# Optimization experiments

Measured on AMD Instinct MI355X. Metric: run time of the kernel, lower is better.

Reference implementation:

```python
import jax, jax.numpy as jnp
import numpy as np

WS = 7
B, Dd, Hh, Wd, C, NH = 1, 28, 28, 28, 384, 12

def _rel_index(ws):
    coords = np.stack(np.meshgrid(np.arange(ws), np.arange(ws), np.arange(ws), indexing='ij'))
    cf = coords.reshape(3, -1)
    rel = (cf[:, :, None] - cf[:, None, :]).transpose(1, 2, 0) + (ws - 1)
    rel[:, :, 0] *= (2 * ws - 1) ** 2
    rel[:, :, 1] *= (2 * ws - 1)
    return rel.sum(-1)  # (ws^3, ws^3)

REL_IDX = _rel_index(WS)

def setup_inputs():
    key = jax.random.key(0)
    ks = jax.random.split(key, 8)
    L = Dd * Hh * Wd
    s = 0.02
    return {
        'skip': jax.random.normal(ks[0], (B, L, C), jnp.float32),
        'x_up': jax.random.normal(ks[1], (B, L, C), jnp.float32),
        'D': Dd, 'H': Hh, 'W': Wd,
        'ln1_g': jnp.ones((C,), jnp.float32), 'ln1_b': jnp.zeros((C,), jnp.float32),
        'kv_w': jax.random.normal(ks[2], (C, 2 * C), jnp.float32) * s,
        'kv_b': jnp.zeros((2 * C,), jnp.float32),
        'rpb': jax.random.normal(ks[3], ((2 * WS - 1) ** 3, NH), jnp.float32) * s,
        'proj_w': jax.random.normal(ks[4], (C, C), jnp.float32) * s,
        'proj_b': jnp.zeros((C,), jnp.float32),
        'ln2_g': jnp.ones((C,), jnp.float32), 'ln2_b': jnp.zeros((C,), jnp.float32),
        'mlp_w1': jax.random.normal(ks[5], (C, 4 * C), jnp.float32) * s,
        'mlp_b1': jnp.zeros((4 * C,), jnp.float32),
        'mlp_w2': jax.random.normal(ks[6], (4 * C, C), jnp.float32) * s,
        'mlp_b2': jnp.zeros((C,), jnp.float32),
    }

def _ln(x, g, b):
    m = jnp.mean(x, -1, keepdims=True)
    v = jnp.mean(jnp.square(x - m), -1, keepdims=True)
    return (x - m) * jax.lax.rsqrt(v + 1e-5) * g + b

def _win_part(x):
    b, d, h, w, c = x.shape
    x = x.reshape(b, d // WS, WS, h // WS, WS, w // WS, WS, c)
    return x.transpose(0, 1, 3, 5, 2, 4, 6, 7).reshape(-1, WS ** 3, c)

def _win_rev(x, b, d, h, w):
    c = x.shape[-1]
    x = x.reshape(b, d // WS, h // WS, w // WS, WS, WS, WS, c)
    return x.transpose(0, 1, 4, 2, 5, 3, 6, 7).reshape(b, d, h, w, c)

def reference(skip, x_up, D, H, W, ln1_g, ln1_b, kv_w, kv_b, rpb, proj_w, proj_b, ln2_g, ln2_b, mlp_w1, mlp_b1, mlp_w2, mlp_b2):
    b, L, c = skip.shape
    x = x_up + skip  # wrapper residual; shortcut of the inner block
    # inner block was built with shift_size=0 -> no cyclic shift, attn_mask unused
    sk = _win_part(_ln(skip, ln1_g, ln1_b).reshape(b, D, H, W, c))   # (nW, N, C) -> K,V source
    qx = _win_part(_ln(x_up, ln1_g, ln1_b).reshape(b, D, H, W, c))   # (nW, N, C) -> Q source
    nW, N, _ = sk.shape
    hd = c // NH
    kv = (sk @ kv_w + kv_b).reshape(nW, N, 2, NH, hd)
    k, v = kv[:, :, 0], kv[:, :, 1]                  # (nW, N, NH, hd)
    q = qx.reshape(nW, N, NH, hd) * (hd ** -0.5)     # no q projection in WindowAttention_kv
    attn = jnp.einsum('wqhd,wkhd->whqk', q, k)
    bias = rpb[REL_IDX.reshape(-1)].reshape(N, N, NH).transpose(2, 0, 1)
    attn = jax.nn.softmax(attn + bias[None], axis=-1)
    o = jnp.einsum('whqk,wkhd->wqhd', attn, v).reshape(nW, N, c)
    o = o @ proj_w + proj_b
    o = _win_rev(o, b, D, H, W).reshape(b, L, c)
    x = x + o
    h1 = jax.nn.gelu(_ln(x, ln2_g, ln2_b) @ mlp_w1 + mlp_b1)
    x = x + h1 @ mlp_w2 + mlp_b2
    return x
```

## Files before the change

kernel.cpp:

```cpp
#include <hip/hip_runtime.h>
#include <hip/hip_bf16.h>
#include <cstdint>

typedef unsigned short u16;
typedef short s16x8 __attribute__((ext_vector_type(8)));
typedef short s16x4 __attribute__((ext_vector_type(4)));
typedef float f32x4 __attribute__((ext_vector_type(4)));

#define C_DIM 384
#define NHEAD 12
#define HD    32
#define NTOK  343
#define NWIN  64
#define LTOT  21952
#define SIDE  28

__device__ __forceinline__ float u2f(u16 u) {
    return __uint_as_float(((unsigned int)u) << 16);
}
__device__ __forceinline__ u16 f2b(float f) {
    unsigned int u = __float_as_uint(f);
    return (u16)((u + 0x7fffu + ((u >> 16) & 1u)) >> 16);
}
__device__ __forceinline__ float exp2_hw(float x) {
    float r;
    asm("v_exp_f32 %0, %1" : "=v"(r) : "v"(x));
    return r;
}
__device__ __forceinline__ unsigned int pk_bf16(float lo, float hi) {
    unsigned int r;
    asm("v_cvt_pk_bf16_f32 %0, %1, %2" : "=v"(r) : "v"(lo), "v"(hi));
    return r;
}
__device__ __forceinline__ float gelu_fast(float x) {
    float e = exp2_hw(-2.3022083f * (x + 0.044715f * x * x * x));
    return x * __builtin_amdgcn_rcpf(1.f + e);
}

__global__ __launch_bounds__(256) void k_wt(
    const float* __restrict__ W, u16* __restrict__ Wt, int K, int N)
{
    __shared__ float T[64][65];
    int k0 = blockIdx.x * 64, n0 = blockIdx.y * 64;
    int t = threadIdx.x;
    int c = t & 63, rg = t >> 6;
#pragma unroll
    for (int i = 0; i < 16; i++) {
        int r = rg * 16 + i;
        T[r][c] = W[(size_t)(k0 + r) * N + n0 + c];
    }
    __syncthreads();
    int k = t & 63, ng = t >> 6;
#pragma unroll
    for (int i = 0; i < 16; i++) {
        int n = ng * 16 + i;
        Wt[(size_t)(n0 + n) * K + k0 + k] = f2b(T[k][n]);
    }
}

__global__ __launch_bounds__(256) void k_wt_pi(
    const float* __restrict__ W, u16* __restrict__ Wt, int K, int N)
{
    __shared__ float T[64][65];
    int k0 = blockIdx.x * 64, n0 = blockIdx.y * 64;
    int t = threadIdx.x;
    int c = t & 63, rg = t >> 6;
#pragma unroll
    for (int i = 0; i < 16; i++) {
        int r = rg * 16 + i;
        T[r][c] = W[(size_t)(k0 + r) * N + n0 + c];
    }
    __syncthreads();
    int k = t & 63, ng = t >> 6;
    int kg = k0 + k;
    int j = kg & 127, ct = j >> 4, nn = j & 15;
    int kp = (kg & ~127) | ((ct >> 1) << 5) | (nn << 1) | (ct & 1);
#pragma unroll
    for (int i = 0; i < 16; i++) {
        int n = ng * 16 + i;
        Wt[(size_t)(n0 + n) * K + kp] = f2b(T[k][n]);
    }
}

__global__ __launch_bounds__(256) void k_bias(
    const float* __restrict__ rpb, u16* __restrict__ biasPl)
{
    int h = blockIdx.x, q = blockIdx.y;
    int qc = min(q, NTOK - 1);
    int qz = qc / 49, qrem = qc % 49, qy = qrem / 7, qx = qrem % 7;
    int cq = qz * 169 + qy * 13 + qx;
    u16* dst = biasPl + ((size_t)h * 352 + q) * 352;
    for (int k = threadIdx.x; k < 352; k += 256) {
        int kc = min(k, NTOK - 1);
        int kz = kc / 49, krem = kc % 49, ky = krem / 7, kx = krem % 7;
        int ck = kz * 169 + ky * 13 + kx;
        dst[k] = f2b(rpb[(size_t)(cq - ck + 1098) * NHEAD + h] * 1.4426950408889634f);
    }
}

#define QSCALE 0.2550348772f

__global__ __launch_bounds__(256) void k_lnprep(
    const float* __restrict__ skip, const float* __restrict__ xup,
    const float* __restrict__ g, const float* __restrict__ bta,
    u16* __restrict__ skW, u16* __restrict__ qW, u16* __restrict__ res)
{
    int t = blockIdx.x * 4 + (threadIdx.x >> 6);
    int lane = threadIdx.x & 63;
    const float* ps = skip + (size_t)t * C_DIM;
    const float* px = xup + (size_t)t * C_DIM;
    float vs[6], vx[6];
    float s1 = 0.f, s2 = 0.f, x1 = 0.f, x2 = 0.f;
#pragma unroll
    for (int j = 0; j < 6; j++) {
        float a = ps[lane + j * 64];
        float b = px[lane + j * 64];
        vs[j] = a; vx[j] = b;
        s1 += a; s2 += a * a; x1 += b; x2 += b * b;
    }
#pragma unroll
    for (int off = 32; off; off >>= 1) {
        s1 += __shfl_xor(s1, off);
        s2 += __shfl_xor(s2, off);
        x1 += __shfl_xor(x1, off);
        x2 += __shfl_xor(x2, off);
    }
    float ms = s1 * (1.f / 384.f), mx = x1 * (1.f / 384.f);
    float rs = rsqrtf(fmaxf(s2 * (1.f / 384.f) - ms * ms, 0.f) + 1e-5f);
    float rx = rsqrtf(fmaxf(x2 * (1.f / 384.f) - mx * mx, 0.f) + 1e-5f);
    int d = t / 784, rem = t % 784, hh = rem / 28, ww = rem % 28;
    int win = (d / 7) * 16 + (hh / 7) * 4 + (ww / 7);
    int n = (d % 7) * 49 + (hh % 7) * 7 + (ww % 7);
    size_t dst = ((size_t)(win * NTOK + n)) * C_DIM + lane;
    size_t td  = (size_t)t * C_DIM + lane;
#pragma unroll
    for (int j = 0; j < 6; j++) {
        int c = lane + j * 64;
        float gg = g[c], bb = bta[c];
        skW[dst + j * 64] = f2b((vs[j] - ms) * rs * gg + bb);
        qW[dst + j * 64]  = f2b(((vx[j] - mx) * rx * gg + bb) * QSCALE);
        res[td + j * 64]  = f2b(vs[j] + vx[j]);
    }
}

__global__ __launch_bounds__(256) void k_ln2(
    const u16* __restrict__ x2, const float* __restrict__ g,
    const float* __restrict__ bta, u16* __restrict__ lnx)
{
    int t = blockIdx.x * 4 + (threadIdx.x >> 6);
    int lane = threadIdx.x & 63;
    const u16* p = x2 + (size_t)t * C_DIM;
    float v[6];
    float s1 = 0.f, s2 = 0.f;
#pragma unroll
    for (int j = 0; j < 6; j++) {
        float a = u2f(p[lane + j * 64]);
        v[j] = a; s1 += a; s2 += a * a;
    }
#pragma unroll
    for (int off = 32; off; off >>= 1) {
        s1 += __shfl_xor(s1, off);
        s2 += __shfl_xor(s2, off);
    }
    float m = s1 * (1.f / 384.f);
    float r = rsqrtf(fmaxf(s2 * (1.f / 384.f) - m * m, 0.f) + 1e-5f);
    size_t dst = (size_t)t * C_DIM + lane;
#pragma unroll
    for (int j = 0; j < 6; j++) {
        int c = lane + j * 64;
        lnx[dst + j * 64] = f2b((v[j] - m) * r * g[c] + bta[c]);
    }
}

#define BPAD 40

__device__ __forceinline__ void gemm128(
    const u16* __restrict__ A, const u16* __restrict__ Bt, int K, int M,
    int rowBase, int colBase, int tid,
    u16 (*As)[BPAD], u16 (*Bs)[BPAD], f32x4 acc[4][4])
{
    const int sr  = tid >> 2;
    const int scg = (tid & 3) << 3;
    const int lane = tid & 63, wv = tid >> 6;
    const int m16 = lane & 15, quad = lane >> 4;
    const int wr = (wv >> 1) << 6, wc = (wv & 1) << 6;

    int ra0 = min(rowBase + sr, M - 1);
    int ra1 = min(rowBase + 64 + sr, M - 1);
    const u16* pa0 = A + (size_t)ra0 * K + scg;
    const u16* pa1 = A + (size_t)ra1 * K + scg;
    const u16* pb0 = Bt + (size_t)(colBase + sr) * K + scg;
    const u16* pb1 = Bt + (size_t)(colBase + 64 + sr) * K + scg;

    uint4 a0 = *(const uint4*)pa0, a1 = *(const uint4*)pa1;
    uint4 b0 = *(const uint4*)pb0, b1 = *(const uint4*)pb1;

    for (int kk = 0; kk < K; kk += 32) {
        *(uint4*)&As[sr][scg]      = a0;
        *(uint4*)&As[64 + sr][scg] = a1;
        *(uint4*)&Bs[sr][scg]      = b0;
        *(uint4*)&Bs[64 + sr][scg] = b1;
        __syncthreads();
        if (kk + 32 < K) {
            a0 = *(const uint4*)(pa0 + kk + 32);
            a1 = *(const uint4*)(pa1 + kk + 32);
            b0 = *(const uint4*)(pb0 + kk + 32);
            b1 = *(const uint4*)(pb1 + kk + 32);
        }
        s16x8 af[4], bf[4];
#pragma unroll
        for (int rt = 0; rt < 4; rt++)
            af[rt] = *(const s16x8*)&As[wr + rt * 16 + m16][quad * 8];
#pragma unroll
        for (int bt = 0; bt < 4; bt++)
            bf[bt] = *(const s16x8*)&Bs[wc + bt * 16 + m16][quad * 8];
#pragma unroll
        for (int rt = 0; rt < 4; rt++)
#pragma unroll
        for (int bt = 0; bt < 4; bt++)
            acc[rt][bt] = __builtin_amdgcn_mfma_f32_16x16x32_bf16(af[rt], bf[bt], acc[rt][bt], 0, 0, 0);
        __syncthreads();
    }
}

__device__ __forceinline__ void gemm64_db(
    const u16* __restrict__ A, const u16* __restrict__ Bt, int K, int M,
    int rowBase, int colBase, int tid,
    u16 (*As)[BPAD], u16 (*Bs)[BPAD], f32x4 acc[4][2])
{
    const int sr  = tid >> 2;
    const int scg = (tid & 3) << 3;
    const int lane = tid & 63, wv = tid >> 6;
    const int m16 = lane & 15, quad = lane >> 4;
    const int wc = wv << 5;

    int ra = min(rowBase + sr, M - 1);
    const u16* pa  = A + (size_t)ra * K + scg;
    const u16* pb0 = Bt + (size_t)(colBase + sr) * K + scg;
    const u16* pb1 = Bt + (size_t)(colBase + 64 + sr) * K + scg;

    uint4 aA = *(const uint4*)pa,        bA0 = *(const uint4*)pb0,        bA1 = *(const uint4*)pb1;
    uint4 aB = *(const uint4*)(pa + 32), bB0 = *(const uint4*)(pb0 + 32), bB1 = *(const uint4*)(pb1 + 32);

    *(uint4*)&As[sr][scg]      = aA;
    *(uint4*)&Bs[sr][scg]      = bA0;
    *(uint4*)&Bs[64 + sr][scg] = bA1;
    if (64 < K) {
        aA  = *(const uint4*)(pa + 64);
        bA0 = *(const uint4*)(pb0 + 64);
        bA1 = *(const uint4*)(pb1 + 64);
    }
    __syncthreads();

    for (int kk = 0; kk < K; kk += 64) {
        *(uint4*)&As[64 + sr][scg]  = aB;
        *(uint4*)&Bs[128 + sr][scg] = bB0;
        *(uint4*)&Bs[192 + sr][scg] = bB1;
        if (kk + 96 < K) {
            aB  = *(const uint4*)(pa  + kk + 96);
            bB0 = *(const uint4*)(pb0 + kk + 96);
            bB1 = *(const uint4*)(pb1 + kk + 96);
        }
        {
            s16x8 af[4], bf[2];
#pragma unroll
            for (int rt = 0; rt < 4; rt++)
                af[rt] = *(const s16x8*)&As[rt * 16 + m16][quad * 8];
#pragma unroll
            for (int bt = 0; bt < 2; bt++)
                bf[bt] = *(const s16x8*)&Bs[wc + bt * 16 + m16][quad * 8];
#pragma unroll
            for (int rt = 0; rt < 4; rt++)
#pragma unroll
            for (int bt = 0; bt < 2; bt++)
                acc[rt][bt] = __builtin_amdgcn_mfma_f32_16x16x32_bf16(af[rt], bf[bt], acc[rt][bt], 0, 0, 0);
        }
        __syncthreads();
        if (kk + 64 < K) {
            *(uint4*)&As[sr][scg]      = aA;
            *(uint4*)&Bs[sr][scg]      = bA0;
            *(uint4*)&Bs[64 + sr][scg] = bA1;
        }
        if (kk + 128 < K) {
            aA  = *(const uint4*)(pa  + kk + 128);
            bA0 = *(const uint4*)(pb0 + kk + 128);
            bA1 = *(const uint4*)(pb1 + kk + 128);
        }
        {
            s16x8 af[4], bf[2];
#pragma unroll
            for (int rt = 0; rt < 4; rt++)
                af[rt] = *(const s16x8*)&As[64 + rt * 16 + m16][quad * 8];
#pragma unroll
            for (int bt = 0; bt < 2; bt++)
                bf[bt] = *(const s16x8*)&Bs[128 + wc + bt * 16 + m16][quad * 8];
#pragma unroll
            for (int rt = 0; rt < 4; rt++)
#pragma unroll
            for (int bt = 0; bt < 2; bt++)
                acc[rt][bt] = __builtin_amdgcn_mfma_f32_16x16x32_bf16(af[rt], bf[bt], acc[rt][bt], 0, 0, 0);
        }
        __syncthreads();
    }
}

#define EPI_SETUP \
    int lane = tid & 63, wv = tid >> 6, quad = lane >> 4, n16 = lane & 15;

__global__ __launch_bounds__(256) void k_gemm_kv(
    const u16* __restrict__ A, const u16* __restrict__ Wt, const float* __restrict__ bias,
    u16* __restrict__ Kb, u16* __restrict__ Vb)
{
    __shared__ __align__(16) u16 As[128][BPAD];
    __shared__ __align__(16) u16 Bs[128][BPAD];
    f32x4 acc[4][4] = {};
    int tid = threadIdx.x;
    int rowBase = blockIdx.x * 128, colBase = blockIdx.y * 128;
    gemm128(A, Wt, 384, LTOT, rowBase, colBase, tid, As, Bs, acc);
    EPI_SETUP
    int wr = (wv >> 1) << 6, wc = (wv & 1) << 6;
#pragma unroll
    for (int bt = 0; bt < 4; bt++) {
        int col = colBase + wc + bt * 16 + n16;
        float bcol = bias[col];
        int isv = col >= 384;
        int remc = col - (isv ? 384 : 0);
        int hh = remc >> 5, dd = remc & 31;
#pragma unroll
        for (int rt = 0; rt < 4; rt++)
#pragma unroll
        for (int reg = 0; reg < 4; reg++) {
            int r = rowBase + wr + rt * 16 + quad * 4 + reg;
            if (r < LTOT) {
                int w = r / NTOK, nn = r % NTOK;
                size_t dst = ((size_t)((w * NHEAD + hh) * NTOK + nn)) * HD + dd;
                (isv ? Vb : Kb)[dst] = f2b(acc[rt][bt][reg] + bcol);
            }
        }
    }
}

__global__ __launch_bounds__(256) void k_gemm_proj(
    const u16* __restrict__ A, const u16* __restrict__ Wt, const float* __restrict__ bias,
    const u16* __restrict__ res, u16* __restrict__ x2)
{
    __shared__ __align__(16) u16 As[128][BPAD];
    __shared__ __align__(16) u16 Bs[256][BPAD];
    f32x4 acc[4][2] = {};
    int tid = threadIdx.x;
    int rowBase = blockIdx.x * 64, colBase = blockIdx.y * 128;
    gemm64_db(A, Wt, 384, LTOT, rowBase, colBase, tid, As, Bs, acc);
    EPI_SETUP
    int wc = wv << 5;
#pragma unroll
    for (int bt = 0; bt < 2; bt++) {
        int col = colBase + wc + bt * 16 + n16;
        float bcol = bias[col];
#pragma unroll
        for (int rt = 0; rt < 4; rt++)
#pragma unroll
        for (int reg = 0; reg < 4; reg++) {
            int r = rowBase + rt * 16 + quad * 4 + reg;
            if (r < LTOT) {
                size_t idx = (size_t)r * C_DIM + col;
                x2[idx] = f2b(acc[rt][bt][reg] + bcol + u2f(res[idx]));
            }
        }
    }
}

__global__ __launch_bounds__(256) void k_gemm_mlp1(
    const u16* __restrict__ A, const u16* __restrict__ Wt, const float* __restrict__ bias,
    u16* __restrict__ h1c, int rowOfs)
{
    __shared__ __align__(16) u16 As[128][BPAD];
    __shared__ __align__(16) u16 Bs[128][BPAD];
    f32x4 acc[4][4] = {};
    int tid = threadIdx.x;
    int rowBase = rowOfs + blockIdx.x * 128, colBase = blockIdx.y * 128;
    gemm128(A, Wt, 384, LTOT, rowBase, colBase, tid, As, Bs, acc);
    EPI_SETUP
    int wr = (wv >> 1) << 6;
#pragma unroll
    for (int p2 = 0; p2 < 2; p2++) {
        int p = (wv & 1) * 2 + p2;
        int col0 = colBase + p * 32 + n16;
        int col1 = col0 + 16;
        float bc0 = bias[col0], bc1 = bias[col1];
        int dcol = colBase + p * 32 + 2 * n16;
#pragma unroll
        for (int rt = 0; rt < 4; rt++)
#pragma unroll
        for (int reg = 0; reg < 4; reg++) {
            int r = rowBase + wr + rt * 16 + quad * 4 + reg;
            if (r < LTOT) {
                size_t rl = (size_t)(r - rowOfs);
                float v0 = gelu_fast(acc[rt][2 * p2][reg] + bc0);
                float v1 = gelu_fast(acc[rt][2 * p2 + 1][reg] + bc1);
                *(unsigned int*)&h1c[rl * 1536 + dcol] = pk_bf16(v0, v1);
            }
        }
    }
}

__global__ __launch_bounds__(256) void k_gemm_mlp2(
    const u16* __restrict__ A, const u16* __restrict__ Wt, const float* __restrict__ bias,
    const u16* __restrict__ x2, float* __restrict__ out, int rowOfs, int chunkRows)
{
    __shared__ __align__(16) u16 As[128][BPAD];
    __shared__ __align__(16) u16 Bs[256][BPAD];
    f32x4 acc[4][2] = {};
    int tid = threadIdx.x;
    int rowBase = blockIdx.x * 64, colBase = blockIdx.y * 128;
    gemm64_db(A, Wt, 1536, chunkRows, rowBase, colBase, tid, As, Bs, acc);
    EPI_SETUP
    int wc = wv << 5;
#pragma unroll
    for (int bt = 0; bt < 2; bt++) {
        int col = colBase + wc + bt * 16 + n16;
        float bcol = bias[col];
#pragma unroll
        for (int rt = 0; rt < 4; rt++)
#pragma unroll
        for (int reg = 0; reg < 4; reg++) {
            int rl = rowBase + rt * 16 + quad * 4 + reg;
            int rg = rowOfs + rl;
            if (rl < chunkRows && rg < LTOT) {
                size_t idx = (size_t)rg * C_DIM + col;
                out[idx] = acc[rt][bt][reg] + bcol + u2f(x2[idx]);
            }
        }
    }
}

#define VP  360
#define PBS 36

__global__ __launch_bounds__(256, 2) void k_attn(
    const u16* __restrict__ qW, const u16* __restrict__ Kb, const u16* __restrict__ Vb,
    const u16* __restrict__ biasPl, u16* __restrict__ oT)
{
    __shared__ __align__(16) u16 Vt[32 * VP];
    __shared__ __align__(16) u16 Pb[4 * 16 * PBS];

    const int h = blockIdx.x, w = blockIdx.y;
    const int tid = threadIdx.x;
    const int lane = tid & 63, wv = tid >> 6;
    const int m16 = lane & 15, quad = lane >> 4;
    const size_t base = ((size_t)(w * NHEAD + h)) * NTOK * HD;
    const u16* Kg = Kb + base;

    for (int t = tid; t < 704; t += 256) {
        int dg = t / 176, rem = t - dg * 176;
        int kb = rem >> 4, j = rem & 15;
        int n0 = kb * 32 + j, n1 = n0 + 16;
        uint4 uA = make_uint4(0, 0, 0, 0), uB = make_uint4(0, 0, 0, 0);
        if (n0 < NTOK) uA = *(const uint4*)(Vb + base + n0 * HD + dg * 8);
        if (n1 < NTOK) uB = *(const uint4*)(Vb + base + n1 * HD + dg * 8);
        int d0 = dg * 8, colu = kb * 32 + 2 * j;
        unsigned int pk0 = (uA.x & 0xffffu) | (uB.x << 16);
        unsigned int pk1 = (uA.x >> 16)     | (uB.x & 0xffff0000u);
        unsigned int pk2 = (uA.y & 0xffffu) | (uB.y << 16);
        unsigned int pk3 = (uA.y >> 16)     | (uB.y & 0xffff0000u);
        unsigned int pk4 = (uA.z & 0xffffu) | (uB.z << 16);
        unsigned int pk5 = (uA.z >> 16)     | (uB.z & 0xffff0000u);
        unsigned int pk6 = (uA.w & 0xffffu) | (uB.w << 16);
        unsigned int pk7 = (uA.w >> 16)     | (uB.w & 0xffff0000u);
        *(unsigned int*)&Vt[(d0 + 0) * VP + colu] = pk0;
        *(unsigned int*)&Vt[(d0 + 1) * VP + colu] = pk1;
        *(unsigned int*)&Vt[(d0 + 2) * VP + colu] = pk2;
        *(unsigned int*)&Vt[(d0 + 3) * VP + colu] = pk3;
        *(unsigned int*)&Vt[(d0 + 4) * VP + colu] = pk4;
        *(unsigned int*)&Vt[(d0 + 5) * VP + colu] = pk5;
        *(unsigned int*)&Vt[(d0 + 6) * VP + colu] = pk6;
        *(unsigned int*)&Vt[(d0 + 7) * VP + colu] = pk7;
    }
    __syncthreads();

    u16* myP = Pb + wv * 16 * PBS;

    for (int qt = wv; qt < 22; qt += 4) {
        int qbase = qt * 16;
        int qrow = min(qbase + m16, NTOK - 1);
        s16x8 qf = *(const s16x8*)(qW + ((size_t)(w * NTOK + qrow)) * C_DIM
                                       + h * HD + quad * 8);
        const u16* bp = biasPl + ((size_t)h * 352 + qbase + quad * 4) * 352;

        f32x4 S0[11], S1[11];
        float mx[4] = {-1e30f, -1e30f, -1e30f, -1e30f};

#pragma unroll
        for (int ks = 0; ks < 11; ks++) {
            int kbase = ks * 32;
            int kt0 = kbase + m16, kt1 = kt0 + 16;
            s16x8 kf0 = *(const s16x8*)(Kg + (size_t)kt0 * HD + quad * 8);
            s16x8 kf1 = *(const s16x8*)(Kg + (size_t)kt1 * HD + quad * 8);
            f32x4 c0, c1;
#pragma unroll
            for (int i = 0; i < 4; i++) {
                c0[i] = u2f(bp[i * 352 + kt0]);
                c1[i] = u2f(bp[i * 352 + kt1]);
            }
            f32x4 sA = __builtin_amdgcn_mfma_f32_16x16x32_bf16(qf, kf0, c0, 0, 0, 0);
            f32x4 sB = __builtin_amdgcn_mfma_f32_16x16x32_bf16(qf, kf1, c1, 0, 0, 0);
            bool k1ok = (ks < 10) || (kt1 < NTOK);
#pragma unroll
            for (int i = 0; i < 4; i++) {
                float sa = sA[i];
                float sb = k1ok ? sB[i] : -1e30f;
                S0[ks][i] = sa;
                S1[ks][i] = sb;
                mx[i] = fmaxf(mx[i], fmaxf(sa, sb));
            }
        }
#pragma unroll
        for (int i = 0; i < 4; i++) {
            float v = mx[i];
            v = fmaxf(v, __shfl_xor(v, 1));
            v = fmaxf(v, __shfl_xor(v, 2));
            v = fmaxf(v, __shfl_xor(v, 4));
            v = fmaxf(v, __shfl_xor(v, 8));
            mx[i] = v;
        }

        f32x4 O0 = {}, O1 = {};
        float l[4] = {};
#pragma unroll
        for (int ks = 0; ks < 11; ks++) {
            int kbase = ks * 32;
#pragma unroll
            for (int i = 0; i < 4; i++) {
                float pa = exp2_hw(S0[ks][i] - mx[i]);
                float pb = exp2_hw(S1[ks][i] - mx[i]);
                l[i] += pa + pb;
                *(unsigned int*)&myP[(quad * 4 + i) * PBS + 2 * m16] = pk_bf16(pa, pb);
            }
            s16x4 plo = *(const s16x4*)&myP[m16 * PBS + quad * 8];
            s16x4 phi = *(const s16x4*)&myP[m16 * PBS + quad * 8 + 4];
            s16x8 pf  = __builtin_shufflevector(plo, phi, 0, 1, 2, 3, 4, 5, 6, 7);
            s16x8 vf0 = *(const s16x8*)&Vt[m16 * VP + kbase + quad * 8];
            s16x8 vf1 = *(const s16x8*)&Vt[(16 + m16) * VP + kbase + quad * 8];
            O0 = __builtin_amdgcn_mfma_f32_16x16x32_bf16(pf, vf0, O0, 0, 0, 0);
            O1 = __builtin_amdgcn_mfma_f32_16x16x32_bf16(pf, vf1, O1, 0, 0, 0);
        }
#pragma unroll
        for (int i = 0; i < 4; i++) {
            float v = l[i];
            v += __shfl_xor(v, 1);
            v += __shfl_xor(v, 2);
            v += __shfl_xor(v, 4);
            v += __shfl_xor(v, 8);
            l[i] = v;
        }

        int wd = w >> 4, wh = (w >> 2) & 3, wwi = w & 3;
#pragma unroll
        for (int i = 0; i < 4; i++) {
            int q = qbase + quad * 4 + i;
            if (q < NTOK) {
                float rl = __builtin_amdgcn_rcpf(l[i]);
                int qz = q / 49, qrem = q % 49, qy = qrem / 7, qx = qrem % 7;
                size_t tok = ((size_t)(wd * 7 + qz) * SIDE + (wh * 7 + qy)) * SIDE
                             + (wwi * 7 + qx);
                u16* op = oT + tok * C_DIM + h * HD;
                op[m16]      = f2b(O0[i] * rl);
                op[16 + m16] = f2b(O1[i] * rl);
            }
        }
    }
}

extern "C" void kernel_launch(void* const* d_in, const int* in_sizes, int n_in,
                              void* d_out, int out_size, void* d_ws, size_t ws_size,
                              hipStream_t stream)
{
    const float* skip = (const float*)d_in[0];
    const float* xup  = (const float*)d_in[1];
    const float* ln1g = (const float*)d_in[5];
    const float* ln1b = (const float*)d_in[6];
    const float* kvw  = (const float*)d_in[7];
    const float* kvb  = (const float*)d_in[8];
    const float* rpb  = (const float*)d_in[9];
    const float* pw   = (const float*)d_in[10];
    const float* pb   = (const float*)d_in[11];
    const float* ln2g = (const float*)d_in[12];
    const float* ln2b = (const float*)d_in[13];
    const float* w1   = (const float*)d_in[14];
    const float* b1   = (const float*)d_in[15];
    const float* w2   = (const float*)d_in[16];
    const float* b2   = (const float*)d_in[17];
    float* out = (float*)d_out;

    char* ws = (char*)d_ws;
    const size_t BUFB = (size_t)LTOT * C_DIM * 2;
    const size_t WTB  = 589824 + 294912 + 1179648 + 1179648;
    const size_t BIASB = (size_t)NHEAD * 352 * 352 * 2;
    u16* skW = (u16*)(ws);
    u16* qW  = (u16*)(ws + BUFB);
    u16* Kb  = (u16*)(ws + 2 * BUFB);
    u16* Vb  = (u16*)(ws + 3 * BUFB);
    u16* oT  = (u16*)(ws);
    u16* x2  = (u16*)(ws + BUFB);
    u16* lnx = (u16*)(ws + 2 * BUFB);
    char* wt = ws + 4 * BUFB;
    u16* kvWt = (u16*)(wt);
    u16* pWt  = (u16*)(wt + 589824);
    u16* w1t  = (u16*)(wt + 589824 + 294912);
    u16* w2t  = (u16*)(wt + 589824 + 294912 + 1179648);
    u16* biasPl = (u16*)(wt + WTB);
    u16* res  = (u16*)d_out;

    const size_t used = 4 * BUFB + WTB + BIASB;
    const size_t blkBytes = 128 * 1536 * 2;
    size_t tailCap = (ws_size > used) ? (ws_size - used) / blkBytes : 0;
    int chunkBlocks;
    u16* h1c;
    if (tailCap >= 43) {
        chunkBlocks = tailCap < 172 ? (int)tailCap : 172;
        h1c = (u16*)(ws + used);
    } else {
        chunkBlocks = 42;
        h1c = (u16*)(ws + 3 * BUFB);
    }

    k_wt<<<dim3(6, 12), 256, 0, stream>>>(kvw, kvWt, 384, 768);
    k_wt<<<dim3(6, 6),  256, 0, stream>>>(pw,  pWt,  384, 384);
    k_wt<<<dim3(6, 24), 256, 0, stream>>>(w1,  w1t,  384, 1536);
    k_wt_pi<<<dim3(24, 6), 256, 0, stream>>>(w2, w2t, 1536, 384);
    k_bias<<<dim3(NHEAD, 352), 256, 0, stream>>>(rpb, biasPl);

    k_lnprep<<<LTOT / 4, 256, 0, stream>>>(skip, xup, ln1g, ln1b, skW, qW, res);
    k_gemm_kv<<<dim3(172, 6), 256, 0, stream>>>(skW, kvWt, kvb, Kb, Vb);
    k_attn<<<dim3(NHEAD, NWIN), 256, 0, stream>>>(qW, Kb, Vb, biasPl, oT);
    k_gemm_proj<<<dim3(343, 3), 256, 0, stream>>>(oT, pWt, pb, res, x2);
    k_ln2<<<LTOT / 4, 256, 0, stream>>>(x2, ln2g, ln2b, lnx);
    for (int b0 = 0; b0 < 172; b0 += chunkBlocks) {
        int nb = (172 - b0) < chunkBlocks ? (172 - b0) : chunkBlocks;
        int rowOfs = b0 * 128;
        int chunkRows = nb * 128;
        if (rowOfs + chunkRows > LTOT) chunkRows = LTOT - rowOfs;
        int nb64 = (chunkRows + 63) / 64;
        k_gemm_mlp1<<<dim3(nb, 12), 256, 0, stream>>>(lnx, w1t, b1, h1c, rowOfs);
        k_gemm_mlp2<<<dim3(nb64, 3), 256, 0, stream>>>(h1c, w2t, b2, x2, out, rowOfs, chunkRows);
    }
}
```

Baseline: 423.1 us.

## Stage GEMM tiles via direct global-to-LDS loads with double buffering

```diff
diff --git a/kernel.cpp b/kernel.cpp
--- a/kernel.cpp
+++ b/kernel.cpp
@@ -35,6 +35,11 @@
 __device__ __forceinline__ float gelu_fast(float x) {
     float e = exp2_hw(-2.3022083f * (x + 0.044715f * x * x * x));
     return x * __builtin_amdgcn_rcpf(1.f + e);
+}
+__device__ __forceinline__ void gl16(const u16* g, u16* l) {
+    __builtin_amdgcn_global_load_lds(
+        (const __attribute__((address_space(1))) void*)g,
+        (__attribute__((address_space(3))) void*)l, 16, 0, 0);
 }
 
 __global__ __launch_bounds__(256) void k_wt(
@@ -172,12 +177,10 @@
     }
 }
 
-#define BPAD 40
-
-__device__ __forceinline__ void gemm128(
+__device__ __forceinline__ void gemm128_gl(
     const u16* __restrict__ A, const u16* __restrict__ Bt, int K, int M,
     int rowBase, int colBase, int tid,
-    u16 (*As)[BPAD], u16 (*Bs)[BPAD], f32x4 acc[4][4])
+    u16 (*As)[32], u16 (*Bs)[32], f32x4 acc[4][4])
 {
     const int sr  = tid >> 2;
     const int scg = (tid & 3) << 3;
@@ -192,41 +195,44 @@
     const u16* pb0 = Bt + (size_t)(colBase + sr) * K + scg;
     const u16* pb1 = Bt + (size_t)(colBase + 64 + sr) * K + scg;
 
-    uint4 a0 = *(const uint4*)pa0, a1 = *(const uint4*)pa1;
-    uint4 b0 = *(const uint4*)pb0, b1 = *(const uint4*)pb1;
-
+    u16* a0d = &As[0][0]  + wv * 512;
+    u16* a1d = &As[64][0] + wv * 512;
+    u16* b0d = &Bs[0][0]  + wv * 512;
+    u16* b1d = &Bs[64][0] + wv * 512;
+
+    gl16(pa0, a0d); gl16(pa1, a1d); gl16(pb0, b0d); gl16(pb1, b1d);
+    __syncthreads();
+
+    int buf = 0;
     for (int kk = 0; kk < K; kk += 32) {
-        *(uint4*)&As[sr][scg]      = a0;
-        *(uint4*)&As[64 + sr][scg] = a1;
-        *(uint4*)&Bs[sr][scg]      = b0;
-        *(uint4*)&Bs[64 + sr][scg] = b1;
-        __syncthreads();
         if (kk + 32 < K) {
-            a0 = *(const uint4*)(pa0 + kk + 32);
-            a1 = *(const uint4*)(pa1 + kk + 32);
-            b0 = *(const uint4*)(pb0 + kk + 32);
-            b1 = *(const uint4*)(pb1 + kk + 32);
+            int nb = (buf ^ 1) * 4096;
+            gl16(pa0 + kk + 32, a0d + nb);
+            gl16(pa1 + kk + 32, a1d + nb);
+            gl16(pb0 + kk + 32, b0d + nb);
+            gl16(pb1 + kk + 32, b1d + nb);
         }
         s16x8 af[4], bf[4];
 #pragma unroll
         for (int rt = 0; rt < 4; rt++)
-            af[rt] = *(const s16x8*)&As[wr + rt * 16 + m16][quad * 8];
+            af[rt] = *(const s16x8*)&As[buf * 128 + wr + rt * 16 + m16][quad * 8];
 #pragma unroll
         for (int bt = 0; bt < 4; bt++)
-            bf[bt] = *(const s16x8*)&Bs[wc + bt * 16 + m16][quad * 8];
+            bf[bt] = *(const s16x8*)&Bs[buf * 128 + wc + bt * 16 + m16][quad * 8];
 #pragma unroll
         for (int rt = 0; rt < 4; rt++)
 #pragma unroll
         for (int bt = 0; bt < 4; bt++)
             acc[rt][bt] = __builtin_amdgcn_mfma_f32_16x16x32_bf16(af[rt], bf[bt], acc[rt][bt], 0, 0, 0);
         __syncthreads();
-    }
-}
-
-__device__ __forceinline__ void gemm64_db(
+        buf ^= 1;
+    }
+}
+
+__device__ __forceinline__ void gemm64_gl(
     const u16* __restrict__ A, const u16* __restrict__ Bt, int K, int M,
     int rowBase, int colBase, int tid,
-    u16 (*As)[BPAD], u16 (*Bs)[BPAD], f32x4 acc[4][2])
+    u16 (*As)[32], u16 (*Bs)[32], f32x4 acc[4][2])
 {
     const int sr  = tid >> 2;
     const int scg = (tid & 3) << 3;
@@ -239,68 +245,36 @@
     const u16* pb0 = Bt + (size_t)(colBase + sr) * K + scg;
     const u16* pb1 = Bt + (size_t)(colBase + 64 + sr) * K + scg;
 
-    uint4 aA = *(const uint4*)pa,        bA0 = *(const uint4*)pb0,        bA1 = *(const uint4*)pb1;
-    uint4 aB = *(const uint4*)(pa + 32), bB0 = *(const uint4*)(pb0 + 32), bB1 = *(const uint4*)(pb1 + 32);
-
-    *(uint4*)&As[sr][scg]      = aA;
-    *(uint4*)&Bs[sr][scg]      = bA0;
-    *(uint4*)&Bs[64 + sr][scg] = bA1;
-    if (64 < K) {
-        aA  = *(const uint4*)(pa + 64);
-        bA0 = *(const uint4*)(pb0 + 64);
-        bA1 = *(const uint4*)(pb1 + 64);
-    }
+    u16* ad  = &As[0][0]  + wv * 512;
+    u16* b0d = &Bs[0][0]  + wv * 512;
+    u16* b1d = &Bs[64][0] + wv * 512;
+
+    gl16(pa, ad); gl16(pb0, b0d); gl16(pb1, b1d);
     __syncthreads();
 
-    for (int kk = 0; kk < K; kk += 64) {
-        *(uint4*)&As[64 + sr][scg]  = aB;
-        *(uint4*)&Bs[128 + sr][scg] = bB0;
-        *(uint4*)&Bs[192 + sr][scg] = bB1;
-        if (kk + 96 < K) {
-            aB  = *(const uint4*)(pa  + kk + 96);
-            bB0 = *(const uint4*)(pb0 + kk + 96);
-            bB1 = *(const uint4*)(pb1 + kk + 96);
-        }
-        {
-            s16x8 af[4], bf[2];
-#pragma unroll
-            for (int rt = 0; rt < 4; rt++)
-                af[rt] = *(const s16x8*)&As[rt * 16 + m16][quad * 8];
-#pragma unroll
-            for (int bt = 0; bt < 2; bt++)
-                bf[bt] = *(const s16x8*)&Bs[wc + bt * 16 + m16][quad * 8];
-#pragma unroll
-            for (int rt = 0; rt < 4; rt++)
-#pragma unroll
-            for (int bt = 0; bt < 2; bt++)
-                acc[rt][bt] = __builtin_amdgcn_mfma_f32_16x16x32_bf16(af[rt], bf[bt], acc[rt][bt], 0, 0, 0);
-        }
+    int buf = 0;
+    for (int kk = 0; kk < K; kk += 32) {
+        if (kk + 32 < K) {
+            int nbA = (buf ^ 1) * 2048;
+            int nbB = (buf ^ 1) * 4096;
+            gl16(pa  + kk + 32, ad  + nbA);
+            gl16(pb0 + kk + 32, b0d + nbB);
+            gl16(pb1 + kk + 32, b1d + nbB);
+        }
+        s16x8 af[4], bf[2];
+#pragma unroll
+        for (int rt = 0; rt < 4; rt++)
+            af[rt] = *(const s16x8*)&As[buf * 64 + rt * 16 + m16][quad * 8];
+#pragma unroll
+        for (int bt = 0; bt < 2; bt++)
+            bf[bt] = *(const s16x8*)&Bs[buf * 128 + wc + bt * 16 + m16][quad * 8];
+#pragma unroll
+        for (int rt = 0; rt < 4; rt++)
+#pragma unroll
+        for (int bt = 0; bt < 2; bt++)
+            acc[rt][bt] = __builtin_amdgcn_mfma_f32_16x16x32_bf16(af[rt], bf[bt], acc[rt][bt], 0, 0, 0);
         __syncthreads();
-        if (kk + 64 < K) {
-            *(uint4*)&As[sr][scg]      = aA;
-            *(uint4*)&Bs[sr][scg]      = bA0;
-            *(uint4*)&Bs[64 + sr][scg] = bA1;
-        }
-        if (kk + 128 < K) {
-            aA  = *(const uint4*)(pa  + kk + 128);
-            bA0 = *(const uint4*)(pb0 + kk + 128);
-            bA1 = *(const uint4*)(pb1 + kk + 128);
-        }
-        {
-            s16x8 af[4], bf[2];
-#pragma unroll
-            for (int rt = 0; rt < 4; rt++)
-                af[rt] = *(const s16x8*)&As[64 + rt * 16 + m16][quad * 8];
-#pragma unroll
-            for (int bt = 0; bt < 2; bt++)
-                bf[bt] = *(const s16x8*)&Bs[128 + wc + bt * 16 + m16][quad * 8];
-#pragma unroll
-            for (int rt = 0; rt < 4; rt++)
-#pragma unroll
-            for (int bt = 0; bt < 2; bt++)
-                acc[rt][bt] = __builtin_amdgcn_mfma_f32_16x16x32_bf16(af[rt], bf[bt], acc[rt][bt], 0, 0, 0);
-        }
-        __syncthreads();
+        buf ^= 1;
     }
 }
 
@@ -311,12 +285,12 @@
     const u16* __restrict__ A, const u16* __restrict__ Wt, const float* __restrict__ bias,
     u16* __restrict__ Kb, u16* __restrict__ Vb)
 {
-    __shared__ __align__(16) u16 As[128][BPAD];
-    __shared__ __align__(16) u16 Bs[128][BPAD];
+    __shared__ __align__(16) u16 As[256][32];
+    __shared__ __align__(16) u16 Bs[256][32];
     f32x4 acc[4][4] = {};
     int tid = threadIdx.x;
     int rowBase = blockIdx.x * 128, colBase = blockIdx.y * 128;
-    gemm128(A, Wt, 384, LTOT, rowBase, colBase, tid, As, Bs, acc);
+    gemm128_gl(A, Wt, 384, LTOT, rowBase, colBase, tid, As, Bs, acc);
     EPI_SETUP
     int wr = (wv >> 1) << 6, wc = (wv & 1) << 6;
 #pragma unroll
@@ -344,12 +318,12 @@
     const u16* __restrict__ A, const u16* __restrict__ Wt, const float* __restrict__ bias,
     const u16* __restrict__ res, u16* __restrict__ x2)
 {
-    __shared__ __align__(16) u16 As[128][BPAD];
-    __shared__ __align__(16) u16 Bs[256][BPAD];
+    __shared__ __align__(16) u16 As[128][32];
+    __shared__ __align__(16) u16 Bs[256][32];
     f32x4 acc[4][2] = {};
     int tid = threadIdx.x;
     int rowBase = blockIdx.x * 64, colBase = blockIdx.y * 128;
-    gemm64_db(A, Wt, 384, LTOT, rowBase, colBase, tid, As, Bs, acc);
+    gemm64_gl(A, Wt, 384, LTOT, rowBase, colBase, tid, As, Bs, acc);
     EPI_SETUP
     int wc = wv << 5;
 #pragma unroll
@@ -373,12 +347,12 @@
     const u16* __restrict__ A, const u16* __restrict__ Wt, const float* __restrict__ bias,
     u16* __restrict__ h1c, int rowOfs)
 {
-    __shared__ __align__(16) u16 As[128][BPAD];
-    __shared__ __align__(16) u16 Bs[128][BPAD];
+    __shared__ __align__(16) u16 As[256][32];
+    __shared__ __align__(16) u16 Bs[256][32];
     f32x4 acc[4][4] = {};
     int tid = threadIdx.x;
     int rowBase = rowOfs + blockIdx.x * 128, colBase = blockIdx.y * 128;
-    gemm128(A, Wt, 384, LTOT, rowBase, colBase, tid, As, Bs, acc);
+    gemm128_gl(A, Wt, 384, LTOT, rowBase, colBase, tid, As, Bs, acc);
     EPI_SETUP
     int wr = (wv >> 1) << 6;
 #pragma unroll
@@ -407,18 +381,25 @@
     const u16* __restrict__ A, const u16* __restrict__ Wt, const float* __restrict__ bias,
     const u16* __restrict__ x2, float* __restrict__ out, int rowOfs, int chunkRows)
 {
-    __shared__ __align__(16) u16 As[128][BPAD];
-    __shared__ __align__(16) u16 Bs[256][BPAD];
+    __shared__ __align__(16) u16 As[128][32];
+    __shared__ __align__(16) u16 Bs[256][32];
     f32x4 acc[4][2] = {};
     int tid = threadIdx.x;
-    int rowBase = blockIdx.x * 64, colBase = blockIdx.y * 128;
-    gemm64_db(A, Wt, 1536, chunkRows, rowBase, colBase, tid, As, Bs, acc);
+    int row = blockIdx.x, col = blockIdx.y;
+    if (gridDim.x == 343) {
+        int v = blockIdx.y * 343 + blockIdx.x;
+        int g = v / 24, i = v % 24;
+        if (g < 42) { row = g * 8 + (i & 7); col = i >> 3; }
+        else        { row = 336 + i % 7;     col = i / 7;  }
+    }
+    int rowBase = row * 64, colBase = col * 128;
+    gemm64_gl(A, Wt, 1536, chunkRows, rowBase, colBase, tid, As, Bs, acc);
     EPI_SETUP
     int wc = wv << 5;
 #pragma unroll
     for (int bt = 0; bt < 2; bt++) {
-        int col = colBase + wc + bt * 16 + n16;
-        float bcol = bias[col];
+        int c2 = colBase + wc + bt * 16 + n16;
+        float bcol = bias[c2];
 #pragma unroll
         for (int rt = 0; rt < 4; rt++)
 #pragma unroll
@@ -426,7 +407,7 @@
             int rl = rowBase + rt * 16 + quad * 4 + reg;
             int rg = rowOfs + rl;
             if (rl < chunkRows && rg < LTOT) {
-                size_t idx = (size_t)rg * C_DIM + col;
+                size_t idx = (size_t)rg * C_DIM + c2;
                 out[idx] = acc[rt][bt][reg] + bcol + u2f(x2[idx]);
             }
         }
```

After: 410.9 us. 2.9% less time.
